# Kernel tuning notes

Hardware: AMD Instinct MI355X
Metric: run time of the kernel (lower is better)

Reference implementation:

```python
import jax, jax.numpy as jnp
import numpy as np

N, E = 20000, 160000
D_IN, HID, HEADS = 256, 64, 10
NEG_SLOPE = 0.2


def setup_inputs() -> dict:
    key = jax.random.key(0)
    ks = jax.random.split(key, 12)
    s = 0.05
    f = jnp.float32
    return {
        "x": jax.random.normal(ks[0], (N, D_IN), f),
        "edge_index": jax.random.randint(ks[1], (2, E), 0, N, jnp.int32),
        # GATConv 1: in=D_IN, out=HID, heads=10, concat=True
        "W1": (jax.random.normal(ks[2], (D_IN, HEADS * HID), f) * s),
        "a_src1": (jax.random.normal(ks[3], (HEADS, HID), f) * s),
        "a_dst1": (jax.random.normal(ks[4], (HEADS, HID), f) * s),
        "b1": jnp.zeros((HEADS * HID,), f),
        # GATConv 2: in=HEADS*HID, out=HID, heads=1
        "W2": (jax.random.normal(ks[5], (HEADS * HID, HID), f) * s),
        "a_src2": (jax.random.normal(ks[6], (1, HID), f) * s),
        "a_dst2": (jax.random.normal(ks[7], (1, HID), f) * s),
        "b2": jnp.zeros((HID,), f),
        # final Linear(hidden_dim, hidden_dim)
        "Wfc": (jax.random.normal(ks[8], (HID, HID), f) * s),
        "bfc": jnp.zeros((HID,), f),
    }


def gat_conv(x, src, dst, n, W, a_src, a_dst, b, heads, concat):
    """PyG GATConv (eval mode): gather, leaky-relu scores, segment softmax, scatter."""
    c = W.shape[1] // heads
    h = (x @ W).reshape(n, heads, c)                      # [N, H, C]
    score_src = jnp.sum(h * a_src, axis=-1)               # [N, H]
    score_dst = jnp.sum(h * a_dst, axis=-1)               # [N, H]
    e = jax.nn.leaky_relu(score_src[src] + score_dst[dst], NEG_SLOPE)  # [E, H]
    # segment softmax over incoming edges of each dst node
    m = jax.ops.segment_max(e, dst, num_segments=n)
    e = jnp.exp(e - m[dst])
    denom = jax.ops.segment_sum(e, dst, num_segments=n)
    alpha = e / (denom[dst] + 1e-16)                      # [E, H]
    msg = alpha[:, :, None] * h[src]                      # [E, H, C]
    out = jax.ops.segment_sum(msg, dst, num_segments=n)   # [N, H, C]
    out = out.reshape(n, heads * c) if concat else out.mean(axis=1)
    return out + b


def reference(x, edge_index, W1, a_src1, a_dst1, b1, W2, a_src2, a_dst2, b2, Wfc, bfc):
    n = x.shape[0]
    # add self loops (PyG default)
    loops = jnp.arange(n, dtype=edge_index.dtype)
    src = jnp.concatenate([edge_index[0], loops])
    dst = jnp.concatenate([edge_index[1], loops])
    h = jax.nn.relu(gat_conv(x, src, dst, n, W1, a_src1, a_dst1, b1, HEADS, True))
    h = jax.nn.relu(gat_conv(h, src, dst, n, W2, a_src2, a_dst2, b2, 1, True))
    return jax.nn.relu(h @ Wfc + bfc)
```

## Files before the change

### kernel.cpp

```cpp
#include <hip/hip_runtime.h>
#include <cstdint>
#include <cstddef>

constexpr int N_NODES = 20000;
constexpr int E_EDGES = 160000;
constexpr int D_INC   = 256;
constexpr int HEADSC  = 10;
constexpr int EN      = E_EDGES + N_NODES;
constexpr int ELLW    = 96;
constexpr float NEG_SLOPE = 0.2f;

typedef _Float16 half8 __attribute__((ext_vector_type(8)));
typedef _Float16 half4v __attribute__((ext_vector_type(4)));
typedef float f32x4 __attribute__((ext_vector_type(4)));

#define GLOBAL_AS const __attribute__((address_space(1))) void*
#define LDS_AS __attribute__((address_space(3))) void*

__global__ __launch_bounds__(256) void gemm1_k(
    const _Float16* __restrict__ A,
    const _Float16* __restrict__ BT,
    _Float16* __restrict__ C,
    const float* __restrict__ asv, const float* __restrict__ adv,
    float* __restrict__ s_s, float* __restrict__ s_d, int M)
{
    __shared__ alignas(16) _Float16 Ah[64][64];
    __shared__ alignas(16) _Float16 Bh[320][64];
    const int tid = threadIdx.x;
    const int wv  = tid >> 6;
    const int ln  = tid & 63;
    const int row0 = blockIdx.y * 64;
    const int col0 = blockIdx.x * 320;
    const int m = ln & 15;
    const int q = ln >> 4;
    const int ar = ln >> 3;
    const int ac = (ln & 7) * 8;

    f32x4 acc[20] = {};

    for (int k0 = 0; k0 < 256; k0 += 64) {
        const _Float16* gp0 = A + (size_t)(row0 + wv * 16 + ar) * 256 + k0 + ac;
        __builtin_amdgcn_global_load_lds((GLOBAL_AS)gp0,
                                         (LDS_AS)&Ah[wv * 16][0], 16, 0, 0);
        __builtin_amdgcn_global_load_lds((GLOBAL_AS)(gp0 + 8 * 256),
                                         (LDS_AS)&Ah[wv * 16 + 8][0], 16, 0, 0);
        const _Float16* gb = BT + (size_t)(col0 + wv * 80 + ar) * 256 + k0 + ac;
#pragma unroll
        for (int jj = 0; jj < 10; ++jj) {
            __builtin_amdgcn_global_load_lds((GLOBAL_AS)(gb + (size_t)jj * 8 * 256),
                                             (LDS_AS)&Bh[wv * 80 + jj * 8][0],
                                             16, 0, 0);
        }
        __syncthreads();
#pragma unroll
        for (int ks = 0; ks < 2; ++ks) {
            const half8 af = *reinterpret_cast<const half8*>(
                &Ah[wv * 16 + m][ks * 32 + q * 8]);
#pragma unroll
            for (int ct = 0; ct < 20; ++ct) {
                const half8 bf = *reinterpret_cast<const half8*>(
                    &Bh[ct * 16 + m][ks * 32 + q * 8]);
                acc[ct] = __builtin_amdgcn_mfma_f32_16x16x32_f16(af, bf, acc[ct],
                                                                 0, 0, 0);
            }
        }
        __syncthreads();
    }

#pragma unroll
    for (int ct = 0; ct < 20; ++ct) {
#pragma unroll
        for (int r = 0; r < 4; ++r) {
            const int row = row0 + wv * 16 + q * 4 + r;
            if (row < M)
                C[(size_t)row * 640 + col0 + ct * 16 + m] = (_Float16)acc[ct][r];
        }
    }

    const int h0 = blockIdx.x * 5;
    float pa[5][4] = {}, pd[5][4] = {};
#pragma unroll
    for (int ct = 0; ct < 20; ++ct) {
        const int hh = ct >> 2;
        const int ch = (ct & 3) * 16 + m;
        const float a_ = asv[(h0 + hh) * 64 + ch];
        const float d_ = adv[(h0 + hh) * 64 + ch];
#pragma unroll
        for (int r = 0; r < 4; ++r) {
            pa[hh][r] += acc[ct][r] * a_;
            pd[hh][r] += acc[ct][r] * d_;
        }
    }
#pragma unroll
    for (int o = 1; o < 16; o <<= 1) {
#pragma unroll
        for (int hh = 0; hh < 5; ++hh)
#pragma unroll
            for (int r = 0; r < 4; ++r) {
                pa[hh][r] += __shfl_xor(pa[hh][r], o, 64);
                pd[hh][r] += __shfl_xor(pd[hh][r], o, 64);
            }
    }
    if (m == 0) {
#pragma unroll
        for (int hh = 0; hh < 5; ++hh)
#pragma unroll
            for (int r = 0; r < 4; ++r) {
                const int row = row0 + wv * 16 + q * 4 + r;
                if (row < M) {
                    s_s[row * HEADSC + h0 + hh] = pa[hh][r];
                    s_d[row * HEADSC + h0 + hh] = pd[hh][r];
                }
            }
    }
}

__global__ __launch_bounds__(256) void gemm2_k(
    const _Float16* __restrict__ A,
    const _Float16* __restrict__ BT,
    _Float16* __restrict__ C,
    const float* __restrict__ asv, const float* __restrict__ adv,
    float* __restrict__ s_s, float* __restrict__ s_d, int M)
{
    __shared__ alignas(16) _Float16 Ah[64][64];
    __shared__ alignas(16) _Float16 Bh[64][64];
    const int tid = threadIdx.x;
    const int wv  = tid >> 6;
    const int ln  = tid & 63;
    const int row0 = blockIdx.x * 64;
    const int m = ln & 15;
    const int q = ln >> 4;
    const int ar = ln >> 3;
    const int ac = (ln & 7) * 8;

    f32x4 acc[4] = {};

    for (int k0 = 0; k0 < 640; k0 += 64) {
        const _Float16* gp0 = A + (size_t)(row0 + wv * 16 + ar) * 640 + k0 + ac;
        __builtin_amdgcn_global_load_lds((GLOBAL_AS)gp0,
                                         (LDS_AS)&Ah[wv * 16][0], 16, 0, 0);
        __builtin_amdgcn_global_load_lds((GLOBAL_AS)(gp0 + 8 * 640),
                                         (LDS_AS)&Ah[wv * 16 + 8][0], 16, 0, 0);
        const _Float16* gb = BT + (size_t)(wv * 16 + ar) * 640 + k0 + ac;
        __builtin_amdgcn_global_load_lds((GLOBAL_AS)gb,
                                         (LDS_AS)&Bh[wv * 16][0], 16, 0, 0);
        __builtin_amdgcn_global_load_lds((GLOBAL_AS)(gb + 8 * 640),
                                         (LDS_AS)&Bh[wv * 16 + 8][0], 16, 0, 0);
        __syncthreads();
#pragma unroll
        for (int ks = 0; ks < 2; ++ks) {
            const half8 af = *reinterpret_cast<const half8*>(
                &Ah[wv * 16 + m][ks * 32 + q * 8]);
#pragma unroll
            for (int ct = 0; ct < 4; ++ct) {
                const half8 bf = *reinterpret_cast<const half8*>(
                    &Bh[ct * 16 + m][ks * 32 + q * 8]);
                acc[ct] = __builtin_amdgcn_mfma_f32_16x16x32_f16(af, bf, acc[ct],
                                                                 0, 0, 0);
            }
        }
        __syncthreads();
    }

#pragma unroll
    for (int ct = 0; ct < 4; ++ct) {
#pragma unroll
        for (int r = 0; r < 4; ++r) {
            const int row = row0 + wv * 16 + q * 4 + r;
            if (row < M)
                C[(size_t)row * 64 + ct * 16 + m] = (_Float16)acc[ct][r];
        }
    }

    float pa[4] = {}, pd[4] = {};
#pragma unroll
    for (int ct = 0; ct < 4; ++ct) {
        const float a_ = asv[ct * 16 + m];
        const float d_ = adv[ct * 16 + m];
#pragma unroll
        for (int r = 0; r < 4; ++r) {
            pa[r] += acc[ct][r] * a_;
            pd[r] += acc[ct][r] * d_;
        }
    }
#pragma unroll
    for (int o = 1; o < 16; o <<= 1) {
#pragma unroll
        for (int r = 0; r < 4; ++r) {
            pa[r] += __shfl_xor(pa[r], o, 64);
            pd[r] += __shfl_xor(pd[r], o, 64);
        }
    }
    if (m == 0) {
#pragma unroll
        for (int r = 0; r < 4; ++r) {
            const int row = row0 + wv * 16 + q * 4 + r;
            if (row < M) { s_s[row] = pa[r]; s_d[row] = pd[r]; }
        }
    }
}

constexpr int XQ   = N_NODES * D_INC / 4;
constexpr int W1E  = D_INC * 640;
constexpr int W2E  = 640 * 64;
constexpr int WFCE = 64 * 64;
constexpr int SETUP_TOT = EN + XQ + W1E + W2E + WFCE;

__global__ void setup_k(const int* __restrict__ src, const int* __restrict__ dst,
                        int* __restrict__ deg, int* __restrict__ ell,
                        const float* __restrict__ x, const float* __restrict__ W1,
                        const float* __restrict__ W2, const float* __restrict__ Wfc,
                        _Float16* __restrict__ x16, _Float16* __restrict__ W1T,
                        _Float16* __restrict__ W2T, _Float16* __restrict__ WfcT)
{
    const int i = blockIdx.x * 256 + threadIdx.x;
    if (i < EN) {
        const int base = deg[N_NODES];
        int d, s;
        if (i < E_EDGES) { d = dst[i]; s = src[i]; }
        else             { d = i - E_EDGES; s = d; }
        const int r = atomicAdd(&deg[d], 1) - base;
        if ((unsigned)r < (unsigned)ELLW) ell[(size_t)d * ELLW + r] = s;
    } else if (i < EN + XQ) {
        const int j = i - EN;
        const float4 v = reinterpret_cast<const float4*>(x)[j];
        half4v o = {(_Float16)v.x, (_Float16)v.y, (_Float16)v.z, (_Float16)v.w};
        reinterpret_cast<half4v*>(x16)[j] = o;
    } else if (i < EN + XQ + W1E) {
        const int j = i - EN - XQ;
        const int k = j / 640, n = j - k * 640;
        W1T[(size_t)n * D_INC + k] = (_Float16)W1[j];
    } else if (i < EN + XQ + W1E + W2E) {
        const int j = i - EN - XQ - W1E;
        const int k = j / 64, n = j - k * 64;
        W2T[(size_t)n * 640 + k] = (_Float16)W2[j];
    } else if (i < SETUP_TOT) {
        const int j = i - EN - XQ - W1E - W2E;
        const int k = j >> 6, n = j & 63;
        WfcT[(size_t)n * 64 + k] = (_Float16)Wfc[j];
    }
}

__global__ __launch_bounds__(320) void agg_f16_oct(
    const _Float16* __restrict__ h, const float* __restrict__ s_s,
    const float* __restrict__ s_d, const int* __restrict__ deg,
    const int* __restrict__ ell, const float* __restrict__ bias,
    _Float16* __restrict__ outp)
{
    const int t   = blockIdx.x * 320 + threadIdx.x;
    const int n   = t / 80;
    const int oct = t - n * 80;
    if (n >= N_NODES) return;
    const int hh  = oct >> 3;
    const _Float16* __restrict__ hb = h + oct * 8;
    const int* __restrict__ row = ell + (size_t)n * ELLW;
    const float sd = s_d[n * HEADSC + hh];
    const int dbase = deg[N_NODES];
    const int dc = min(deg[n] - dbase, ELLW);

    float acc[8] = {};
    float den = 0.f;
    int i = 0;
    for (; i + 7 < dc; i += 8) {
        int   sv[8];
        float gv[8];
        half8 hv[8];
#pragma unroll
        for (int u = 0; u < 8; ++u) sv[u] = row[i + u];
#pragma unroll
        for (int u = 0; u < 8; ++u) gv[u] = s_s[sv[u] * HEADSC + hh];
#pragma unroll
        for (int u = 0; u < 8; ++u)
            hv[u] = *reinterpret_cast<const half8*>(hb + (size_t)sv[u] * 640);
#pragma unroll
        for (int u = 0; u < 8; ++u) {
            float e = gv[u] + sd;
            e = (e > 0.f) ? e : NEG_SLOPE * e;
            const float w = __expf(e);
            den += w;
#pragma unroll
            for (int j = 0; j < 8; ++j) acc[j] += w * (float)hv[u][j];
        }
    }
    for (; i + 3 < dc; i += 4) {
        int   sv[4];
        float gv[4];
        half8 hv[4];
#pragma unroll
        for (int u = 0; u < 4; ++u) sv[u] = row[i + u];
#pragma unroll
        for (int u = 0; u < 4; ++u) gv[u] = s_s[sv[u] * HEADSC + hh];
#pragma unroll
        for (int u = 0; u < 4; ++u)
            hv[u] = *reinterpret_cast<const half8*>(hb + (size_t)sv[u] * 640);
#pragma unroll
        for (int u = 0; u < 4; ++u) {
            float e = gv[u] + sd;
            e = (e > 0.f) ? e : NEG_SLOPE * e;
            const float w = __expf(e);
            den += w;
#pragma unroll
            for (int j = 0; j < 8; ++j) acc[j] += w * (float)hv[u][j];
        }
    }
    for (; i < dc; ++i) {
        const int s0 = row[i];
        const float g0 = s_s[s0 * HEADSC + hh];
        const half8 v0 = *reinterpret_cast<const half8*>(hb + (size_t)s0 * 640);
        float e0 = g0 + sd;
        e0 = (e0 > 0.f) ? e0 : NEG_SLOPE * e0;
        const float w0 = __expf(e0);
        den += w0;
#pragma unroll
        for (int j = 0; j < 8; ++j) acc[j] += w0 * (float)v0[j];
    }
    const float inv = 1.f / (den + 1e-16f);
    const float* bb = bias + oct * 8;
    half8 o;
#pragma unroll
    for (int j = 0; j < 8; ++j)
        o[j] = (_Float16)fmaxf(acc[j] * inv + bb[j], 0.f);
    *reinterpret_cast<half8*>(outp + (size_t)n * 640 + oct * 8) = o;
}

__global__ __launch_bounds__(256) void agg2fc_k(
    const _Float16* __restrict__ h,
    const float* __restrict__ s_s, const float* __restrict__ s_d,
    const int* __restrict__ deg, const int* __restrict__ ell,
    const float* __restrict__ b2,
    const _Float16* __restrict__ WfcT,
    const float* __restrict__ bfc,
    float* __restrict__ out)
{
    __shared__ alignas(16) _Float16 Os[32][72];
    const int tid = threadIdx.x;
    const int n0  = blockIdx.x * 32;
    const int nl  = tid >> 3;
    const int oct = tid & 7;
    const int n   = n0 + nl;

    {
        const _Float16* __restrict__ hb = h + oct * 8;
        const int* __restrict__ row = ell + (size_t)n * ELLW;
        const float sd = s_d[n];
        const int dbase = deg[N_NODES];
        const int dc = min(deg[n] - dbase, ELLW);

        float acc[8] = {};
        float den = 0.f;
        int i = 0;
        for (; i + 3 < dc; i += 4) {
            int   sv[4];
            float gv[4];
            half8 hv[4];
#pragma unroll
            for (int u = 0; u < 4; ++u) sv[u] = row[i + u];
#pragma unroll
            for (int u = 0; u < 4; ++u) gv[u] = s_s[sv[u]];
#pragma unroll
            for (int u = 0; u < 4; ++u)
                hv[u] = *reinterpret_cast<const half8*>(hb + (size_t)sv[u] * 64);
#pragma unroll
            for (int u = 0; u < 4; ++u) {
                float e = gv[u] + sd;
                e = (e > 0.f) ? e : NEG_SLOPE * e;
                const float w = __expf(e);
                den += w;
#pragma unroll
                for (int j = 0; j < 8; ++j) acc[j] += w * (float)hv[u][j];
            }
        }
        for (; i < dc; ++i) {
            const int s0 = row[i];
            const float g0 = s_s[s0];
            const half8 v0 = *reinterpret_cast<const half8*>(hb + (size_t)s0 * 64);
            float e0 = g0 + sd;
            e0 = (e0 > 0.f) ? e0 : NEG_SLOPE * e0;
            const float w0 = __expf(e0);
            den += w0;
#pragma unroll
            for (int j = 0; j < 8; ++j) acc[j] += w0 * (float)v0[j];
        }
        const float inv = 1.f / (den + 1e-16f);
        const float* bb = b2 + oct * 8;
        half8 o;
#pragma unroll
        for (int j = 0; j < 8; ++j)
            o[j] = (_Float16)fmaxf(acc[j] * inv + bb[j], 0.f);
        *reinterpret_cast<half8*>(&Os[nl][oct * 8]) = o;
    }
    __syncthreads();

    const int wv = tid >> 6;
    const int ln = tid & 63;
    if (wv < 2) {
        const int m = ln & 15;
        const int q = ln >> 4;
        f32x4 acc[4] = {};
#pragma unroll
        for (int ks = 0; ks < 2; ++ks) {
            const half8 af = *reinterpret_cast<const half8*>(
                &Os[wv * 16 + m][ks * 32 + q * 8]);
#pragma unroll
            for (int ct = 0; ct < 4; ++ct) {
                const half8 bf = *reinterpret_cast<const half8*>(
                    WfcT + (size_t)(ct * 16 + m) * 64 + ks * 32 + q * 8);
                acc[ct] = __builtin_amdgcn_mfma_f32_16x16x32_f16(af, bf, acc[ct],
                                                                 0, 0, 0);
            }
        }
#pragma unroll
        for (int ct = 0; ct < 4; ++ct) {
#pragma unroll
            for (int r = 0; r < 4; ++r) {
                const int row = n0 + wv * 16 + q * 4 + r;
                const int col = ct * 16 + m;
                out[(size_t)row * 64 + col] = fmaxf(acc[ct][r] + bfc[col], 0.f);
            }
        }
    }
}

extern "C" void kernel_launch(void* const* d_in, const int* in_sizes, int n_in,
                              void* d_out, int out_size, void* d_ws, size_t ws_size,
                              hipStream_t stream)
{
    const float* x      = (const float*)d_in[0];
    const int*   edges  = (const int*)d_in[1];
    const float* W1     = (const float*)d_in[2];
    const float* a_src1 = (const float*)d_in[3];
    const float* a_dst1 = (const float*)d_in[4];
    const float* b1     = (const float*)d_in[5];
    const float* W2     = (const float*)d_in[6];
    const float* a_src2 = (const float*)d_in[7];
    const float* a_dst2 = (const float*)d_in[8];
    const float* b2     = (const float*)d_in[9];
    const float* Wfc    = (const float*)d_in[10];
    const float* bfc    = (const float*)d_in[11];
    float* out = (float*)d_out;

    const int* src = edges;
    const int* dst = edges + E_EDGES;

    char* ws = (char*)d_ws;
    size_t off = 0;
    auto alloc = [&](size_t bytes) -> void* {
        void* p = ws + off;
        off += (bytes + 255) & ~(size_t)255;
        return p;
    };
    _Float16*  h1     = (_Float16*)alloc((size_t)N_NODES * 640 * sizeof(_Float16));
    _Float16*  out1   = (_Float16*)alloc((size_t)N_NODES * 640 * sizeof(_Float16));
    _Float16*  h2     = (_Float16*)alloc((size_t)N_NODES * 64 * sizeof(_Float16));
    _Float16*  x16    = (_Float16*)alloc((size_t)N_NODES * D_INC * sizeof(_Float16));
    _Float16*  W1T    = (_Float16*)alloc((size_t)640 * D_INC * sizeof(_Float16));
    _Float16*  W2T    = (_Float16*)alloc((size_t)64 * 640 * sizeof(_Float16));
    _Float16*  WfcT   = (_Float16*)alloc((size_t)64 * 64 * sizeof(_Float16));
    float*     s_src1 = (float*)alloc((size_t)N_NODES * HEADSC * sizeof(float));
    float*     s_dst1 = (float*)alloc((size_t)N_NODES * HEADSC * sizeof(float));
    float*     s_src2 = (float*)alloc((size_t)N_NODES * sizeof(float));
    float*     s_dst2 = (float*)alloc((size_t)N_NODES * sizeof(float));
    int*       deg    = (int*)alloc((size_t)(N_NODES + 1) * sizeof(int));
    int*       ell    = (int*)alloc((size_t)N_NODES * ELLW * sizeof(int));

    setup_k<<<(SETUP_TOT + 255) / 256, 256, 0, stream>>>(
        src, dst, deg, ell, x, W1, W2, Wfc, x16, W1T, W2T, WfcT);

    dim3 g1(2, (N_NODES + 63) / 64);
    gemm1_k<<<g1, 256, 0, stream>>>(x16, W1T, h1, a_src1, a_dst1,
                                    s_src1, s_dst1, N_NODES);

    agg_f16_oct<<<(N_NODES * 80) / 320, 320, 0, stream>>>(h1, s_src1, s_dst1, deg,
                                                          ell, b1, out1);

    gemm2_k<<<(N_NODES + 63) / 64, 256, 0, stream>>>(out1, W2T, h2,
                                                     a_src2, a_dst2,
                                                     s_src2, s_dst2, N_NODES);

    agg2fc_k<<<N_NODES / 32, 256, 0, stream>>>(h2, s_src2, s_dst2, deg, ell,
                                               b2, WfcT, bfc, out);
}
```

Before: 199.5 us.

## Fuse x fp16 conversion into GEMM1, retile columns, simplify aggregation unroll

GEMM1 now reads fp32 x directly, converts it to fp16 in registers and stores it to padded LDS, so the separate x16 conversion pass in setup and its buffer are removed. The column tile shrinks from 320 to 128 (grid 5 wide), which lowers accumulator register pressure but re-reads the A tile more often. The layer-1 aggregation drops its 8-wide unroll for a flat 4-wide body with pairwise sums and is split into two launches of half the nodes each. The extra launch and the repeated A loads add overhead in exchange for fewer setup bytes and more GEMM blocks.

```diff
diff --git a/kernel.cpp b/kernel.cpp
--- a/kernel.cpp
+++ b/kernel.cpp
@@ -18,37 +18,48 @@
 #define LDS_AS __attribute__((address_space(3))) void*
 
 __global__ __launch_bounds__(256) void gemm1_k(
-    const _Float16* __restrict__ A,
+    const float* __restrict__ X,
     const _Float16* __restrict__ BT,
     _Float16* __restrict__ C,
     const float* __restrict__ asv, const float* __restrict__ adv,
     float* __restrict__ s_s, float* __restrict__ s_d, int M)
 {
-    __shared__ alignas(16) _Float16 Ah[64][64];
-    __shared__ alignas(16) _Float16 Bh[320][64];
+    __shared__ alignas(16) _Float16 Ah[64][68];
+    __shared__ alignas(16) _Float16 Bh[128][64];
     const int tid = threadIdx.x;
     const int wv  = tid >> 6;
     const int ln  = tid & 63;
     const int row0 = blockIdx.y * 64;
-    const int col0 = blockIdx.x * 320;
+    const int col0 = blockIdx.x * 128;
     const int m = ln & 15;
     const int q = ln >> 4;
     const int ar = ln >> 3;
     const int ac = (ln & 7) * 8;
-
-    f32x4 acc[20] = {};
+    const int arow = tid >> 2;
+    const int acg  = (tid & 3) * 16;
+
+    f32x4 acc[8] = {};
 
     for (int k0 = 0; k0 < 256; k0 += 64) {
-        const _Float16* gp0 = A + (size_t)(row0 + wv * 16 + ar) * 256 + k0 + ac;
-        __builtin_amdgcn_global_load_lds((GLOBAL_AS)gp0,
-                                         (LDS_AS)&Ah[wv * 16][0], 16, 0, 0);
-        __builtin_amdgcn_global_load_lds((GLOBAL_AS)(gp0 + 8 * 256),
-                                         (LDS_AS)&Ah[wv * 16 + 8][0], 16, 0, 0);
-        const _Float16* gb = BT + (size_t)(col0 + wv * 80 + ar) * 256 + k0 + ac;
-#pragma unroll
-        for (int jj = 0; jj < 10; ++jj) {
+        float4 v0 = make_float4(0.f, 0.f, 0.f, 0.f), v1 = v0, v2 = v0, v3 = v0;
+        if (row0 + arow < M) {
+            const float* xp = X + (size_t)(row0 + arow) * 256 + k0 + acg;
+            v0 = *reinterpret_cast<const float4*>(xp);
+            v1 = *reinterpret_cast<const float4*>(xp + 4);
+            v2 = *reinterpret_cast<const float4*>(xp + 8);
+            v3 = *reinterpret_cast<const float4*>(xp + 12);
+        }
+        half8 h0 = {(_Float16)v0.x, (_Float16)v0.y, (_Float16)v0.z, (_Float16)v0.w,
+                    (_Float16)v1.x, (_Float16)v1.y, (_Float16)v1.z, (_Float16)v1.w};
+        half8 h1v = {(_Float16)v2.x, (_Float16)v2.y, (_Float16)v2.z, (_Float16)v2.w,
+                     (_Float16)v3.x, (_Float16)v3.y, (_Float16)v3.z, (_Float16)v3.w};
+        *reinterpret_cast<half8*>(&Ah[arow][acg])     = h0;
+        *reinterpret_cast<half8*>(&Ah[arow][acg + 8]) = h1v;
+        const _Float16* gb = BT + (size_t)(col0 + wv * 32 + ar) * 256 + k0 + ac;
+#pragma unroll
+        for (int jj = 0; jj < 4; ++jj) {
             __builtin_amdgcn_global_load_lds((GLOBAL_AS)(gb + (size_t)jj * 8 * 256),
-                                             (LDS_AS)&Bh[wv * 80 + jj * 8][0],
+                                             (LDS_AS)&Bh[wv * 32 + jj * 8][0],
                                              16, 0, 0);
         }
         __syncthreads();
@@ -57,7 +68,7 @@
             const half8 af = *reinterpret_cast<const half8*>(
                 &Ah[wv * 16 + m][ks * 32 + q * 8]);
 #pragma unroll
-            for (int ct = 0; ct < 20; ++ct) {
+            for (int ct = 0; ct < 8; ++ct) {
                 const half8 bf = *reinterpret_cast<const half8*>(
                     &Bh[ct * 16 + m][ks * 32 + q * 8]);
                 acc[ct] = __builtin_amdgcn_mfma_f32_16x16x32_f16(af, bf, acc[ct],
@@ -68,7 +79,7 @@
     }
 
 #pragma unroll
-    for (int ct = 0; ct < 20; ++ct) {
+    for (int ct = 0; ct < 8; ++ct) {
 #pragma unroll
         for (int r = 0; r < 4; ++r) {
             const int row = row0 + wv * 16 + q * 4 + r;
@@ -77,14 +88,14 @@
         }
     }
 
-    const int h0 = blockIdx.x * 5;
-    float pa[5][4] = {}, pd[5][4] = {};
-#pragma unroll
-    for (int ct = 0; ct < 20; ++ct) {
+    const int h0i = blockIdx.x * 2;
+    float pa[2][4] = {}, pd[2][4] = {};
+#pragma unroll
+    for (int ct = 0; ct < 8; ++ct) {
         const int hh = ct >> 2;
         const int ch = (ct & 3) * 16 + m;
-        const float a_ = asv[(h0 + hh) * 64 + ch];
-        const float d_ = adv[(h0 + hh) * 64 + ch];
+        const float a_ = asv[(h0i + hh) * 64 + ch];
+        const float d_ = adv[(h0i + hh) * 64 + ch];
 #pragma unroll
         for (int r = 0; r < 4; ++r) {
             pa[hh][r] += acc[ct][r] * a_;
@@ -94,7 +105,7 @@
 #pragma unroll
     for (int o = 1; o < 16; o <<= 1) {
 #pragma unroll
-        for (int hh = 0; hh < 5; ++hh)
+        for (int hh = 0; hh < 2; ++hh)
 #pragma unroll
             for (int r = 0; r < 4; ++r) {
                 pa[hh][r] += __shfl_xor(pa[hh][r], o, 64);
@@ -103,13 +114,13 @@
     }
     if (m == 0) {
 #pragma unroll
-        for (int hh = 0; hh < 5; ++hh)
+        for (int hh = 0; hh < 2; ++hh)
 #pragma unroll
             for (int r = 0; r < 4; ++r) {
                 const int row = row0 + wv * 16 + q * 4 + r;
                 if (row < M) {
-                    s_s[row * HEADSC + h0 + hh] = pa[hh][r];
-                    s_d[row * HEADSC + h0 + hh] = pd[hh][r];
+                    s_s[row * HEADSC + h0i + hh] = pa[hh][r];
+                    s_d[row * HEADSC + h0i + hh] = pd[hh][r];
                 }
             }
     }
@@ -200,18 +211,17 @@
     }
 }
 
-constexpr int XQ   = N_NODES * D_INC / 4;
 constexpr int W1E  = D_INC * 640;
 constexpr int W2E  = 640 * 64;
 constexpr int WFCE = 64 * 64;
-constexpr int SETUP_TOT = EN + XQ + W1E + W2E + WFCE;
+constexpr int SETUP_TOT = EN + W1E + W2E + WFCE;
 
 __global__ void setup_k(const int* __restrict__ src, const int* __restrict__ dst,
                         int* __restrict__ deg, int* __restrict__ ell,
-                        const float* __restrict__ x, const float* __restrict__ W1,
-                        const float* __restrict__ W2, const float* __restrict__ Wfc,
-                        _Float16* __restrict__ x16, _Float16* __restrict__ W1T,
-                        _Float16* __restrict__ W2T, _Float16* __restrict__ WfcT)
+                        const float* __restrict__ W1, const float* __restrict__ W2,
+                        const float* __restrict__ Wfc,
+                        _Float16* __restrict__ W1T, _Float16* __restrict__ W2T,
+                        _Float16* __restrict__ WfcT)
 {
     const int i = blockIdx.x * 256 + threadIdx.x;
     if (i < EN) {
@@ -221,21 +231,16 @@
         else             { d = i - E_EDGES; s = d; }
         const int r = atomicAdd(&deg[d], 1) - base;
         if ((unsigned)r < (unsigned)ELLW) ell[(size_t)d * ELLW + r] = s;
-    } else if (i < EN + XQ) {
+    } else if (i < EN + W1E) {
         const int j = i - EN;
-        const float4 v = reinterpret_cast<const float4*>(x)[j];
-        half4v o = {(_Float16)v.x, (_Float16)v.y, (_Float16)v.z, (_Float16)v.w};
-        reinterpret_cast<half4v*>(x16)[j] = o;
-    } else if (i < EN + XQ + W1E) {
-        const int j = i - EN - XQ;
         const int k = j / 640, n = j - k * 640;
         W1T[(size_t)n * D_INC + k] = (_Float16)W1[j];
-    } else if (i < EN + XQ + W1E + W2E) {
-        const int j = i - EN - XQ - W1E;
+    } else if (i < EN + W1E + W2E) {
+        const int j = i - EN - W1E;
         const int k = j / 64, n = j - k * 64;
         W2T[(size_t)n * 640 + k] = (_Float16)W2[j];
     } else if (i < SETUP_TOT) {
-        const int j = i - EN - XQ - W1E - W2E;
+        const int j = i - EN - W1E - W2E;
         const int k = j >> 6, n = j & 63;
         WfcT[(size_t)n * 64 + k] = (_Float16)Wfc[j];
     }
@@ -245,11 +250,11 @@
     const _Float16* __restrict__ h, const float* __restrict__ s_s,
     const float* __restrict__ s_d, const int* __restrict__ deg,
     const int* __restrict__ ell, const float* __restrict__ bias,
-    _Float16* __restrict__ outp)
+    _Float16* __restrict__ outp, int n_base)
 {
     const int t   = blockIdx.x * 320 + threadIdx.x;
-    const int n   = t / 80;
-    const int oct = t - n * 80;
+    const int n   = n_base + t / 80;
+    const int oct = t - (t / 80) * 80;
     if (n >= N_NODES) return;
     const int hh  = oct >> 3;
     const _Float16* __restrict__ hb = h + oct * 8;
@@ -261,47 +266,26 @@
     float acc[8] = {};
     float den = 0.f;
     int i = 0;
-    for (; i + 7 < dc; i += 8) {
-        int   sv[8];
-        float gv[8];
-        half8 hv[8];
-#pragma unroll
-        for (int u = 0; u < 8; ++u) sv[u] = row[i + u];
-#pragma unroll
-        for (int u = 0; u < 8; ++u) gv[u] = s_s[sv[u] * HEADSC + hh];
-#pragma unroll
-        for (int u = 0; u < 8; ++u)
-            hv[u] = *reinterpret_cast<const half8*>(hb + (size_t)sv[u] * 640);
-#pragma unroll
-        for (int u = 0; u < 8; ++u) {
-            float e = gv[u] + sd;
-            e = (e > 0.f) ? e : NEG_SLOPE * e;
-            const float w = __expf(e);
-            den += w;
-#pragma unroll
-            for (int j = 0; j < 8; ++j) acc[j] += w * (float)hv[u][j];
-        }
-    }
     for (; i + 3 < dc; i += 4) {
-        int   sv[4];
-        float gv[4];
-        half8 hv[4];
-#pragma unroll
-        for (int u = 0; u < 4; ++u) sv[u] = row[i + u];
-#pragma unroll
-        for (int u = 0; u < 4; ++u) gv[u] = s_s[sv[u] * HEADSC + hh];
-#pragma unroll
-        for (int u = 0; u < 4; ++u)
-            hv[u] = *reinterpret_cast<const half8*>(hb + (size_t)sv[u] * 640);
-#pragma unroll
-        for (int u = 0; u < 4; ++u) {
-            float e = gv[u] + sd;
-            e = (e > 0.f) ? e : NEG_SLOPE * e;
-            const float w = __expf(e);
-            den += w;
-#pragma unroll
-            for (int j = 0; j < 8; ++j) acc[j] += w * (float)hv[u][j];
-        }
+        const int s0 = row[i], s1 = row[i + 1], s2 = row[i + 2], s3 = row[i + 3];
+        const float g0 = s_s[s0 * HEADSC + hh], g1 = s_s[s1 * HEADSC + hh];
+        const float g2 = s_s[s2 * HEADSC + hh], g3 = s_s[s3 * HEADSC + hh];
+        const half8 v0 = *reinterpret_cast<const half8*>(hb + (size_t)s0 * 640);
+        const half8 v1 = *reinterpret_cast<const half8*>(hb + (size_t)s1 * 640);
+        const half8 v2 = *reinterpret_cast<const half8*>(hb + (size_t)s2 * 640);
+        const half8 v3 = *reinterpret_cast<const half8*>(hb + (size_t)s3 * 640);
+        float e0 = g0 + sd, e1 = g1 + sd, e2 = g2 + sd, e3 = g3 + sd;
+        e0 = (e0 > 0.f) ? e0 : NEG_SLOPE * e0;
+        e1 = (e1 > 0.f) ? e1 : NEG_SLOPE * e1;
+        e2 = (e2 > 0.f) ? e2 : NEG_SLOPE * e2;
+        e3 = (e3 > 0.f) ? e3 : NEG_SLOPE * e3;
+        const float w0 = __expf(e0), w1 = __expf(e1);
+        const float w2 = __expf(e2), w3 = __expf(e3);
+        den += (w0 + w1) + (w2 + w3);
+#pragma unroll
+        for (int j = 0; j < 8; ++j)
+            acc[j] += (w0 * (float)v0[j] + w1 * (float)v1[j])
+                    + (w2 * (float)v2[j] + w3 * (float)v3[j]);
     }
     for (; i < dc; ++i) {
         const int s0 = row[i];
@@ -452,7 +436,6 @@
     _Float16*  h1     = (_Float16*)alloc((size_t)N_NODES * 640 * sizeof(_Float16));
     _Float16*  out1   = (_Float16*)alloc((size_t)N_NODES * 640 * sizeof(_Float16));
     _Float16*  h2     = (_Float16*)alloc((size_t)N_NODES * 64 * sizeof(_Float16));
-    _Float16*  x16    = (_Float16*)alloc((size_t)N_NODES * D_INC * sizeof(_Float16));
     _Float16*  W1T    = (_Float16*)alloc((size_t)640 * D_INC * sizeof(_Float16));
     _Float16*  W2T    = (_Float16*)alloc((size_t)64 * 640 * sizeof(_Float16));
     _Float16*  WfcT   = (_Float16*)alloc((size_t)64 * 64 * sizeof(_Float16));
@@ -464,14 +447,16 @@
     int*       ell    = (int*)alloc((size_t)N_NODES * ELLW * sizeof(int));
 
     setup_k<<<(SETUP_TOT + 255) / 256, 256, 0, stream>>>(
-        src, dst, deg, ell, x, W1, W2, Wfc, x16, W1T, W2T, WfcT);
-
-    dim3 g1(2, (N_NODES + 63) / 64);
-    gemm1_k<<<g1, 256, 0, stream>>>(x16, W1T, h1, a_src1, a_dst1,
+        src, dst, deg, ell, W1, W2, Wfc, W1T, W2T, WfcT);
+
+    dim3 g1(5, (N_NODES + 63) / 64);
+    gemm1_k<<<g1, 256, 0, stream>>>(x, W1T, h1, a_src1, a_dst1,
                                     s_src1, s_dst1, N_NODES);
 
-    agg_f16_oct<<<(N_NODES * 80) / 320, 320, 0, stream>>>(h1, s_src1, s_dst1, deg,
-                                                          ell, b1, out1);
+    agg_f16_oct<<<2500, 320, 0, stream>>>(h1, s_src1, s_dst1, deg, ell, b1,
+                                          out1, 0);
+    agg_f16_oct<<<2500, 320, 0, stream>>>(h1, s_src1, s_dst1, deg, ell, b1,
+                                          out1, 10000);
 
     gemm2_k<<<(N_NODES + 63) / 64, 256, 0, stream>>>(out1, W2T, h2,
                                                      a_src2, a_dst2,
```

Result: no change. 196.4 us (-1.5%).
